# Kernel optimization log

Measured on AMD Instinct MI355X. Metric: run time of the kernel, lower is better.

The kernel has to match this reference:

```python
import jax, jax.numpy as jnp
import numpy as np

# dims: d=1024 model width, h=16 heads, d_head=64
B, S, D, H = 4, 1024, 1024, 16
RD = float(np.sqrt(D))
VAR_W_INIT = 0.001  # var_init[0]: initial weight-variance value


def setup_inputs() -> dict:
    key = jax.random.key(0)
    ks = jax.random.split(key, 5)
    x = jax.random.normal(ks[0], (B, S, D), jnp.float32)
    # input variance must be non-negative; small positive values
    var_x = jax.random.uniform(ks[1], (B, S, D), jnp.float32) * 0.01
    scale = 1.0 / np.sqrt(D)
    Wq = jax.random.normal(ks[2], (D, D), jnp.float32) * scale
    Wk = jax.random.normal(ks[3], (D, D), jnp.float32) * scale
    Wv = jax.random.normal(ks[4], (D, D), jnp.float32) * scale
    var_Wq = jnp.full((D, D), VAR_W_INIT, jnp.float32)
    var_Wk = jnp.full((D, D), VAR_W_INIT, jnp.float32)
    var_Wv = jnp.full((D, D), VAR_W_INIT, jnp.float32)
    return dict(x=x, var_x=var_x, Wq=Wq, var_Wq=var_Wq, Wk=Wk, var_Wk=var_Wk, Wv=Wv, var_Wv=var_Wv)


def _linear_vmp(x, var_x, W, var_W):
    # mean: x W^T ; variance of product of independent Gaussians:
    # var = var_x (W^2)^T + x^2 var_W^T + var_x var_W^T
    m = x @ W.T
    v = var_x @ (W * W).T + (x * x) @ var_W.T + var_x @ var_W.T
    return m, v


def _quadratic_vmp(m1, v1, m2, v2):
    # matmul of two independent Gaussian tensors (moment propagation)
    m = m1 @ m2
    v = v1 @ v2 + v1 @ (m2 * m2) + (m1 * m1) @ v2
    return m, v


def _softmax_vmp(a, var_a):
    # delta-method through softmax: J_ij = s_i(delta_ij - s_j)
    # var_i = s_i^2 [ (1-2 s_i) var_i + sum_j s_j^2 var_j ]
    s = jax.nn.softmax(a, axis=-1)
    sv = jnp.sum(s * s * var_a, axis=-1, keepdims=True)
    var_s = s * s * ((1.0 - 2.0 * s) * var_a + sv)
    return s, var_s


def _split_heads(t):
    b, s, _ = t.shape
    return t.reshape(b, s, H, D // H).transpose(0, 2, 1, 3)  # [B,H,S,dh]


def reference(x, var_x, Wq, var_Wq, Wk, var_Wk, Wv, var_Wv):
    q, vq = _linear_vmp(x, var_x, Wq, var_Wq)
    k, vk = _linear_vmp(x, var_x, Wk, var_Wk)
    v, vv = _linear_vmp(x, var_x, Wv, var_Wv)
    q, vq, k, vk, v, vv = map(_split_heads, (q, vq, k, vk, v, vv))
    kt = k.transpose(0, 1, 3, 2)
    vkt = vk.transpose(0, 1, 3, 2)
    a, va = _quadratic_vmp(q, vq, kt, vkt)          # [B,H,S,S]
    a, va = a / RD, va / (RD * RD)
    a, va = _softmax_vmp(a, va)                      # masking=False path
    o, vo = _quadratic_vmp(a, va, v, vv)             # [B,H,S,dh]
    o = o.transpose(0, 2, 1, 3).reshape(x.shape)
    vo = vo.transpose(0, 2, 1, 3).reshape(x.shape)
    # residual_vmp, mode='identity': mean add, variances add
    return x + o, var_x + vo
```

## Files before the change

kernel.cpp:

```cpp
#include <hip/hip_runtime.h>
#include <hip/hip_bf16.h>

#define BB 4
#define SS 1024
#define DD 1024
#define HH 16
#define DH 64
#define MM (BB*SS)

typedef __attribute__((ext_vector_type(8))) short bf16x8;
typedef __attribute__((ext_vector_type(8))) unsigned short u16x8;
typedef __attribute__((ext_vector_type(4))) float f32x4;

__device__ __forceinline__ float b2f(unsigned short u) {
    union { unsigned int i; float f; } c; c.i = ((unsigned int)u) << 16; return c.f;
}
__device__ __forceinline__ unsigned short f2b(float f) {
    __hip_bfloat16 h = __float2bfloat16(f);
    return *reinterpret_cast<unsigned short*>(&h);
}
__device__ __forceinline__ unsigned int pack2(float a, float b) {
    return (unsigned int)f2b(a) | ((unsigned int)f2b(b) << 16);
}
__device__ __forceinline__ void gload16(const unsigned short* g, unsigned short* l) {
    __builtin_amdgcn_global_load_lds(
        (const __attribute__((address_space(1))) void*)g,
        (__attribute__((address_space(3))) void*)l,
        16, 0, 0);
}
#define MFMA16(a, b, c) __builtin_amdgcn_mfma_f32_16x16x32_bf16(a, b, c, 0, 0, 0)

__global__ __launch_bounds__(256) void prep_x_kernel(
    const float* __restrict__ x, const float* __restrict__ vx,
    unsigned short* __restrict__ xb, unsigned short* __restrict__ vxb,
    unsigned short* __restrict__ xsb)
{
    const size_t i = ((size_t)blockIdx.x * 256 + threadIdx.x) * 4;
    float4 a = *(const float4*)(x + i);
    float4 b = *(const float4*)(vx + i);
    ushort4 oa = { f2b(a.x), f2b(a.y), f2b(a.z), f2b(a.w) };
    ushort4 ob = { f2b(b.x), f2b(b.y), f2b(b.z), f2b(b.w) };
    ushort4 os = { f2b(a.x*a.x), f2b(a.y*a.y), f2b(a.z*a.z), f2b(a.w*a.w) };
    *(ushort4*)(xb  + i) = oa;
    *(ushort4*)(vxb + i) = ob;
    *(ushort4*)(xsb + i) = os;
}

__global__ __launch_bounds__(256) void prep_w_kernel(
    const float* __restrict__ W, const float* __restrict__ vW,
    unsigned short* __restrict__ wb, unsigned short* __restrict__ wc,
    unsigned short* __restrict__ wv)
{
    const size_t i = ((size_t)blockIdx.x * 256 + threadIdx.x) * 4;
    float4 a = *(const float4*)(W + i);
    float4 b = *(const float4*)(vW + i);
    ushort4 oa = { f2b(a.x), f2b(a.y), f2b(a.z), f2b(a.w) };
    ushort4 oc = { f2b(a.x*a.x + b.x), f2b(a.y*a.y + b.y),
                   f2b(a.z*a.z + b.z), f2b(a.w*a.w + b.w) };
    ushort4 ov = { f2b(b.x), f2b(b.y), f2b(b.z), f2b(b.w) };
    *(ushort4*)(wb + i) = oa;
    *(ushort4*)(wc + i) = oc;
    *(ushort4*)(wv + i) = ov;
}

__global__ __launch_bounds__(256) void gemm_mean_kernel(
    const unsigned short* __restrict__ xb,
    const unsigned short* __restrict__ w0b, const unsigned short* __restrict__ w1b,
    const unsigned short* __restrict__ w2b,
    unsigned short* __restrict__ o0m, unsigned short* __restrict__ o1m,
    unsigned short* __restrict__ o2m)
{
    __shared__ unsigned short sA[128*32];
    __shared__ unsigned short sB[128*32];

    const int z = blockIdx.z;
    const unsigned short* Wb = (z==0)? w0b : (z==1)? w1b : w2b;
    unsigned short* Om = (z==0)? o0m : (z==1)? o1m : o2m;

    const int bn = blockIdx.x;
    const int bm = blockIdx.y;
    const int tid = threadIdx.x;
    const int w = tid >> 6;
    const int l = tid & 63;
    const int wr = w >> 1, wc = w & 1;

    const int c0 = w*64 + l;
    const int r0 = c0 >> 2, cc0 = (c0 & 3) * 8;
    const int c1 = c0 + 256;
    const int r1 = c1 >> 2, cc1 = (c1 & 3) * 8;

    const size_t aoff0 = (size_t)(bm*128 + r0) * DD + cc0;
    const size_t aoff1 = (size_t)(bm*128 + r1) * DD + cc1;
    const size_t boff0 = (size_t)(bn*128 + r0) * DD + cc0;
    const size_t boff1 = (size_t)(bn*128 + r1) * DD + cc1;

    const int lb0 = (w*64) * 8;
    const int lb1 = (256 + w*64) * 8;

    f32x4 acc[4][4];
    #pragma unroll
    for (int i = 0; i < 4; ++i)
        #pragma unroll
        for (int j = 0; j < 4; ++j)
            acc[i][j] = (f32x4){0.f,0.f,0.f,0.f};

    const int fr = l & 15;
    const int fk = (l >> 4) << 3;

    for (int kk = 0; kk < DD; kk += 32) {
        gload16(xb + aoff0 + kk, &sA[lb0]);
        gload16(xb + aoff1 + kk, &sA[lb1]);
        gload16(Wb + boff0 + kk, &sB[lb0]);
        gload16(Wb + boff1 + kk, &sB[lb1]);
        __syncthreads();

        bf16x8 bfr[4];
        #pragma unroll
        for (int j = 0; j < 4; ++j)
            bfr[j] = *(const bf16x8*)&sB[(wc*64 + j*16 + fr)*32 + fk];
        #pragma unroll
        for (int i = 0; i < 4; ++i) {
            bf16x8 a0 = *(const bf16x8*)&sA[(wr*64 + i*16 + fr)*32 + fk];
            #pragma unroll
            for (int j = 0; j < 4; ++j)
                acc[i][j] = MFMA16(a0, bfr[j], acc[i][j]);
        }
        __syncthreads();
    }

    const int orow = bm*128 + wr*64 + ((l >> 4) << 2);
    const int ocol = bn*128 + wc*64 + fr;
    #pragma unroll
    for (int i = 0; i < 4; ++i)
        #pragma unroll
        for (int j = 0; j < 4; ++j)
            #pragma unroll
            for (int r = 0; r < 4; ++r)
                Om[(size_t)(orow + i*16 + r) * DD + ocol + j*16] = f2b(acc[i][j][r]);
}

__global__ __launch_bounds__(256) void gemm_var_kernel(
    const unsigned short* __restrict__ vxb, const unsigned short* __restrict__ xsb,
    const unsigned short* __restrict__ w0c, const unsigned short* __restrict__ w0v,
    const unsigned short* __restrict__ w1c, const unsigned short* __restrict__ w1v,
    const unsigned short* __restrict__ w2c, const unsigned short* __restrict__ w2v,
    unsigned short* __restrict__ o0v, unsigned short* __restrict__ o1v,
    unsigned short* __restrict__ o2v)
{
    __shared__ unsigned short sA1[128*32];
    __shared__ unsigned short sA2[128*32];
    __shared__ unsigned short sB1[128*32];
    __shared__ unsigned short sB2[128*32];

    const int z = blockIdx.z;
    const unsigned short* Wc = (z==0)? w0c : (z==1)? w1c : w2c;
    const unsigned short* Wv = (z==0)? w0v : (z==1)? w1v : w2v;
    unsigned short* Ov = (z==0)? o0v : (z==1)? o1v : o2v;

    const int bn = blockIdx.x;
    const int bm = blockIdx.y;
    const int tid = threadIdx.x;
    const int w = tid >> 6;
    const int l = tid & 63;
    const int wr = w >> 1, wc = w & 1;

    const int c0 = w*64 + l;
    const int r0 = c0 >> 2, cc0 = (c0 & 3) * 8;
    const int c1 = c0 + 256;
    const int r1 = c1 >> 2, cc1 = (c1 & 3) * 8;

    const size_t aoff0 = (size_t)(bm*128 + r0) * DD + cc0;
    const size_t aoff1 = (size_t)(bm*128 + r1) * DD + cc1;
    const size_t boff0 = (size_t)(bn*128 + r0) * DD + cc0;
    const size_t boff1 = (size_t)(bn*128 + r1) * DD + cc1;

    const int lb0 = (w*64) * 8;
    const int lb1 = (256 + w*64) * 8;

    f32x4 acc[4][4];
    #pragma unroll
    for (int i = 0; i < 4; ++i)
        #pragma unroll
        for (int j = 0; j < 4; ++j)
            acc[i][j] = (f32x4){0.f,0.f,0.f,0.f};

    const int fr = l & 15;
    const int fk = (l >> 4) << 3;

    for (int kk = 0; kk < DD; kk += 32) {
        gload16(vxb + aoff0 + kk, &sA1[lb0]);
        gload16(vxb + aoff1 + kk, &sA1[lb1]);
        gload16(xsb + aoff0 + kk, &sA2[lb0]);
        gload16(xsb + aoff1 + kk, &sA2[lb1]);
        gload16(Wc + boff0 + kk, &sB1[lb0]);
        gload16(Wc + boff1 + kk, &sB1[lb1]);
        gload16(Wv + boff0 + kk, &sB2[lb0]);
        gload16(Wv + boff1 + kk, &sB2[lb1]);
        __syncthreads();

        bf16x8 bc[4], bv[4];
        #pragma unroll
        for (int j = 0; j < 4; ++j) {
            const int bo = (wc*64 + j*16 + fr)*32 + fk;
            bc[j] = *(const bf16x8*)&sB1[bo];
            bv[j] = *(const bf16x8*)&sB2[bo];
        }
        #pragma unroll
        for (int i = 0; i < 4; ++i) {
            const int ao = (wr*64 + i*16 + fr)*32 + fk;
            bf16x8 a1 = *(const bf16x8*)&sA1[ao];
            bf16x8 a2 = *(const bf16x8*)&sA2[ao];
            #pragma unroll
            for (int j = 0; j < 4; ++j) {
                acc[i][j] = MFMA16(a1, bc[j], acc[i][j]);
                acc[i][j] = MFMA16(a2, bv[j], acc[i][j]);
            }
        }
        __syncthreads();
    }

    const int orow = bm*128 + wr*64 + ((l >> 4) << 2);
    const int ocol = bn*128 + wc*64 + fr;
    #pragma unroll
    for (int i = 0; i < 4; ++i)
        #pragma unroll
        for (int j = 0; j < 4; ++j)
            #pragma unroll
            for (int r = 0; r < 4; ++r)
                Ov[(size_t)(orow + i*16 + r) * DD + ocol + j*16] = f2b(acc[i][j][r]);
}

__global__ __launch_bounds__(256) void prep_vt_kernel(
    const unsigned short* __restrict__ vm, const unsigned short* __restrict__ vvv,
    unsigned short* __restrict__ vt, unsigned short* __restrict__ wt,
    unsigned short* __restrict__ vvt)
{
    __shared__ unsigned short tv[64][68];
    __shared__ unsigned short tw[64][68];
    __shared__ unsigned short tvv[64][68];
    const int t = threadIdx.x;
    const int jt = blockIdx.x, h = blockIdx.y, b = blockIdx.z;
    const size_t ibase = (size_t)b*SS*DD + (size_t)h*DH;
    {
        const int j = t & 63, cg = t >> 6;
        const size_t ga = ibase + (size_t)(jt*64 + j)*DD + cg*16;
        #pragma unroll
        for (int hh = 0; hh < 2; ++hh) {
            u16x8 v8  = *(const u16x8*)(vm  + ga + hh*8);
            u16x8 vv8 = *(const u16x8*)(vvv + ga + hh*8);
            u16x8 w8;
            #pragma unroll
            for (int e = 0; e < 8; ++e) {
                float vf = b2f(v8[e]);
                w8[e] = f2b(b2f(vv8[e]) + vf*vf);
            }
            *(u16x8*)&tv[j][cg*16 + hh*8]  = v8;
            *(u16x8*)&tvv[j][cg*16 + hh*8] = vv8;
            *(u16x8*)&tw[j][cg*16 + hh*8]  = w8;
        }
    }
    __syncthreads();
    {
        const int d  = t >> 2;
        const int pc = t & 3;
        const int lc = pc ^ ((d >> 1) & 3);
        #pragma unroll
        for (int st = 0; st < 2; ++st) {
            u16x8 o0, o1, o2;
            #pragma unroll
            for (int e = 0; e < 8; ++e) {
                const int jl = st*32 + (e >> 2)*16 + lc*4 + (e & 3);
                o0[e] = tv[jl][d];
                o1[e] = tw[jl][d];
                o2[e] = tvv[jl][d];
            }
            const size_t ob = (size_t)((b*HH + h)*DH + d)*SS + jt*64 + st*32 + pc*8;
            *(u16x8*)(vt  + ob) = o0;
            *(u16x8*)(wt  + ob) = o1;
            *(u16x8*)(vvt + ob) = o2;
        }
    }
}

__global__ __launch_bounds__(256) void prep_kk_kernel(
    const unsigned short* __restrict__ kmp, const unsigned short* __restrict__ kvp,
    unsigned short* __restrict__ kkb)
{
    const size_t i = ((size_t)blockIdx.x * 256 + threadIdx.x) * 8;
    u16x8 k8 = *(const u16x8*)(kmp + i);
    u16x8 v8 = *(const u16x8*)(kvp + i);
    u16x8 o8;
    #pragma unroll
    for (int e = 0; e < 8; ++e) {
        float kf = b2f(k8[e]);
        o8[e] = f2b(b2f(v8[e]) + kf*kf);
    }
    *(u16x8*)(kkb + i) = o8;
}

union PW { unsigned int u[4]; bf16x8 v; };

__global__ __launch_bounds__(256, 3) void attn_mfma_kernel(
    const unsigned short* __restrict__ kmg, const unsigned short* __restrict__ kvg,
    const unsigned short* __restrict__ kkg,
    const unsigned short* __restrict__ vtg, const unsigned short* __restrict__ wtg,
    const unsigned short* __restrict__ vvtg,
    const unsigned short* __restrict__ qmg, const unsigned short* __restrict__ qvg,
    const float* __restrict__ x, const float* __restrict__ vx,
    float* __restrict__ om, float* __restrict__ ov)
{
    __shared__ unsigned short Ks[2][3][32*64];
    __shared__ unsigned short Vs[2][3][64*32];

    const int tid = threadIdx.x;
    const int w = tid >> 6, l = tid & 63;
    const int lo = l & 15, hi = l >> 4;

    const int fb = blockIdx.x;
    const int g  = ((fb >> 7) << 3) | (fb & 7);
    const int qt = (fb >> 3) & 15;
    const int h  = g & 15;
    const int b  = g >> 4;

    const size_t xbase = (size_t)b*SS*DD + (size_t)h*DH;
    const size_t vbase = (size_t)(b*HH + h)*DH*SS;

    bf16x8 qA[2], vqA[2], qsA[2];
    {
        const int qrow = qt*64 + w*16 + lo;
        #pragma unroll
        for (int ks = 0; ks < 2; ++ks) {
            const size_t ga = xbase + (size_t)qrow*DD + ks*32 + hi*8;
            qA[ks]  = *(const bf16x8*)(qmg + ga);
            vqA[ks] = *(const bf16x8*)(qvg + ga);
            #pragma unroll
            for (int e = 0; e < 8; ++e) {
                float f = b2f((unsigned short)qA[ks][e]);
                qsA[ks][e] = (short)f2b(f*f);
            }
        }
    }
    bf16x8 onesB;
    #pragma unroll
    for (int e = 0; e < 8; ++e) onesB[e] = (short)0x3F80;

    f32x4 T1[4], T2[4], T3[4], T4[4], T5[4];
    f32x4 zac = {0.f,0.f,0.f,0.f}, e2vac = {0.f,0.f,0.f,0.f};
    #pragma unroll
    for (int cb = 0; cb < 4; ++cb) {
        T1[cb] = (f32x4){0.f,0.f,0.f,0.f};
        T2[cb] = (f32x4){0.f,0.f,0.f,0.f};
        T3[cb] = (f32x4){0.f,0.f,0.f,0.f};
        T4[cb] = (f32x4){0.f,0.f,0.f,0.f};
        T5[cb] = (f32x4){0.f,0.f,0.f,0.f};
    }

    const size_t koff = (size_t)(l >> 3)*DD + (size_t)(((l & 7) ^ ((l >> 3) & 7)) * 8);
    const size_t voff = (size_t)(l >> 2)*SS + (size_t)((l & 3) * 8);

    const float INV_RD  = 0.03125f;
    const float INV_RD2 = 0.0009765625f;

#define IK(bu, m, p, G) gload16(G + xbase + (j0 + (size_t)(p)*8)*DD + koff, &Ks[bu][m][(p)*512])
#define IV(bu, m, p, G) gload16(G + vbase + (size_t)((p)*16)*SS + j0 + voff, &Vs[bu][m][(p)*512])
#define STAGE(tt, bu) do {                                                     \
        const size_t j0 = (size_t)(tt) * 32;                                   \
        if (w == 0)      { IK(bu,0,0,kmg); IK(bu,0,1,kmg); IK(bu,0,2,kmg);     \
                           IK(bu,0,3,kmg); IK(bu,1,0,kvg); IK(bu,1,1,kvg); }   \
        else if (w == 1) { IK(bu,1,2,kvg); IK(bu,1,3,kvg); IK(bu,2,0,kkg);     \
                           IK(bu,2,1,kkg); IK(bu,2,2,kkg); IK(bu,2,3,kkg); }   \
        else if (w == 2) { IV(bu,0,0,vtg); IV(bu,0,1,vtg); IV(bu,0,2,vtg);     \
                           IV(bu,0,3,vtg); IV(bu,1,0,wtg); IV(bu,1,1,wtg); }   \
        else             { IV(bu,1,2,wtg); IV(bu,1,3,wtg); IV(bu,2,0,vvtg);    \
                           IV(bu,2,1,vvtg); IV(bu,2,2,vvtg); IV(bu,2,3,vvtg); }\
    } while (0)

    STAGE(0, 0);
    __syncthreads();

    int cur = 0;
    for (int t = 0; t < SS/32; ++t) {
        if (t + 1 < SS/32) STAGE(t + 1, cur ^ 1);

        PW pe, pe2, pev, pe3;
        #pragma unroll
        for (int jb = 0; jb < 2; ++jb) {
            f32x4 aa = {0.f,0.f,0.f,0.f}, vva = {0.f,0.f,0.f,0.f};
            const int jrow = jb*16 + lo;
            #pragma unroll
            for (int ks = 0; ks < 2; ++ks) {
                const int co = jrow*64 + (((ks*4 + hi) ^ (lo & 7)) * 8);
                bf16x8 kB  = *(const bf16x8*)&Ks[cur][0][co];
                bf16x8 vkB = *(const bf16x8*)&Ks[cur][1][co];
                bf16x8 kkB = *(const bf16x8*)&Ks[cur][2][co];
                aa  = MFMA16(kB,  qA[ks],  aa);
                vva = MFMA16(kkB, vqA[ks], vva);
                vva = MFMA16(vkB, qsA[ks], vva);
            }
            #pragma unroll
            for (int rp = 0; rp < 2; ++rp) {
                float a0 = aa[rp*2]   * INV_RD,  va0 = vva[rp*2]   * INV_RD2;
                float a1 = aa[rp*2+1] * INV_RD,  va1 = vva[rp*2+1] * INV_RD2;
                float e0 = __expf(a0), e1 = __expf(a1);
                float s0 = e0*e0,      s1 = e1*e1;
                float v0 = s0*va0,     v1 = s1*va1;
                float t0 = v0*e0,      t1 = v1*e1;
                pe.u [jb*2+rp] = pack2(e0, e1);
                pe2.u[jb*2+rp] = pack2(s0, s1);
                pev.u[jb*2+rp] = pack2(v0, v1);
                pe3.u[jb*2+rp] = pack2(t0, t1);
            }
        }

        zac   = MFMA16(pe.v,  onesB, zac);
        e2vac = MFMA16(pev.v, onesB, e2vac);
        #pragma unroll
        for (int cb = 0; cb < 4; ++cb) {
            const int vo = (cb*16 + lo)*32 + ((hi ^ ((lo >> 1) & 3)) * 8);
            bf16x8 vB  = *(const bf16x8*)&Vs[cur][0][vo];
            bf16x8 wB  = *(const bf16x8*)&Vs[cur][1][vo];
            bf16x8 vvB = *(const bf16x8*)&Vs[cur][2][vo];
            T1[cb] = MFMA16(pe.v,  vB,  T1[cb]);
            T2[cb] = MFMA16(pev.v, wB,  T2[cb]);
            T3[cb] = MFMA16(pe3.v, wB,  T3[cb]);
            T4[cb] = MFMA16(pe2.v, wB,  T4[cb]);
            T5[cb] = MFMA16(pe2.v, vvB, T5[cb]);
        }

        __syncthreads();
        cur ^= 1;
    }

    #pragma unroll
    for (int r = 0; r < 4; ++r) {
        const float Z     = zac[r];
        const float invZ  = 1.f / Z;
        const float invZ2 = invZ * invZ;
        const float sv    = e2vac[r] * invZ2;
        const int row = qt*64 + w*16 + hi*4 + r;
        #pragma unroll
        for (int cb = 0; cb < 4; ++cb) {
            const size_t gi = xbase + (size_t)row*DD + cb*16 + lo;
            const float o  = T1[cb][r] * invZ;
            const float vo = (T2[cb][r] + sv*T4[cb][r] + T5[cb][r]) * invZ2
                           - 2.f * T3[cb][r] * invZ2 * invZ;
            om[gi] = x[gi] + o;
            ov[gi] = vx[gi] + vo;
        }
    }
#undef IK
#undef IV
#undef STAGE
}

extern "C" void kernel_launch(void* const* d_in, const int* in_sizes, int n_in,
                              void* d_out, int out_size, void* d_ws, size_t ws_size,
                              hipStream_t stream) {
    const float* x    = (const float*)d_in[0];
    const float* vx   = (const float*)d_in[1];
    const float* Wq   = (const float*)d_in[2];
    const float* vWq  = (const float*)d_in[3];
    const float* Wk   = (const float*)d_in[4];
    const float* vWk  = (const float*)d_in[5];
    const float* Wv   = (const float*)d_in[6];
    const float* vWv  = (const float*)d_in[7];

    const size_t NE = (size_t)MM * DD;
    const size_t NW = (size_t)DD * DD;

    unsigned short* u = (unsigned short*)d_ws;
    unsigned short* qm   = u + 0*NE;
    unsigned short* qv   = u + 1*NE;
    unsigned short* km   = u + 2*NE;
    unsigned short* kv   = u + 3*NE;
    unsigned short* vm   = u + 4*NE;
    unsigned short* vvv  = u + 5*NE;
    unsigned short* xbb  = u + 6*NE;
    unsigned short* vxbb = u + 7*NE;
    unsigned short* xsbb = u + 8*NE;
    unsigned short* wp   = u + 9*NE;
    unsigned short* wqb = wp + 0*NW, *wqc = wp + 1*NW, *wqv = wp + 2*NW;
    unsigned short* wkb = wp + 3*NW, *wkc = wp + 4*NW, *wkv = wp + 5*NW;
    unsigned short* wvb = wp + 6*NW, *wvc = wp + 7*NW, *wvv = wp + 8*NW;

    float* om = (float*)d_out;
    float* ov = om + NE;

    prep_x_kernel<<<4096, 256, 0, stream>>>(x, vx, xbb, vxbb, xsbb);
    prep_w_kernel<<<1024, 256, 0, stream>>>(Wq, vWq, wqb, wqc, wqv);
    prep_w_kernel<<<1024, 256, 0, stream>>>(Wk, vWk, wkb, wkc, wkv);
    prep_w_kernel<<<1024, 256, 0, stream>>>(Wv, vWv, wvb, wvc, wvv);

    dim3 gg(8, 32, 3);
    gemm_mean_kernel<<<gg, 256, 0, stream>>>(xbb, wqb, wkb, wvb, qm, km, vm);
    gemm_var_kernel<<<gg, 256, 0, stream>>>(vxbb, xsbb,
        wqc, wqv, wkc, wkv, wvc, wvv, qv, kv, vvv);

    unsigned short* vt  = xbb;
    unsigned short* wt  = vxbb;
    unsigned short* vvt = xsbb;
    unsigned short* kkb = wp;
    dim3 gt(SS/64, HH, BB);
    prep_vt_kernel<<<gt, 256, 0, stream>>>(vm, vvv, vt, wt, vvt);
    prep_kk_kernel<<<2048, 256, 0, stream>>>(km, kv, kkb);

    attn_mfma_kernel<<<1024, 256, 0, stream>>>(km, kv, kkb, vt, wt, vvt,
                                               qm, qv, x, vx, om, ov);
}
```

Before: 245.4 us.

## Merge mean/variance projection GEMMs into one double-buffered swizzled kernel

Replaces the separate mean and variance projection GEMM kernels with a single kernel launched over six z-slices. The variance slices run as one GEMM with a doubled K loop that walks both operand pairs in sequence. The K loop now uses double-buffered LDS so the next tile's global loads overlap the current tile's MFMAs, and an XOR swizzle on LDS columns is meant to reduce bank conflicts. The three weight-prep launches are also merged into one grid, which cuts launch count and lets mean and variance blocks share the GPU, at the cost of uneven block lengths within the grid.

```diff
diff --git a/kernel.cpp b/kernel.cpp
--- a/kernel.cpp
+++ b/kernel.cpp
@@ -47,10 +47,19 @@
 }
 
 __global__ __launch_bounds__(256) void prep_w_kernel(
-    const float* __restrict__ W, const float* __restrict__ vW,
-    unsigned short* __restrict__ wb, unsigned short* __restrict__ wc,
-    unsigned short* __restrict__ wv)
-{
+    const float* __restrict__ W0, const float* __restrict__ vW0,
+    const float* __restrict__ W1, const float* __restrict__ vW1,
+    const float* __restrict__ W2, const float* __restrict__ vW2,
+    unsigned short* __restrict__ wp)
+{
+    const int z = blockIdx.y;
+    const float* W  = (z==0)? W0 : (z==1)? W1 : W2;
+    const float* vW = (z==0)? vW0: (z==1)? vW1: vW2;
+    const size_t NW = (size_t)DD*DD;
+    unsigned short* wb = wp + (size_t)(3*z+0)*NW;
+    unsigned short* wc = wp + (size_t)(3*z+1)*NW;
+    unsigned short* wv = wp + (size_t)(3*z+2)*NW;
+
     const size_t i = ((size_t)blockIdx.x * 256 + threadIdx.x) * 4;
     float4 a = *(const float4*)(W + i);
     float4 b = *(const float4*)(vW + i);
@@ -63,19 +72,29 @@
     *(ushort4*)(wv + i) = ov;
 }
 
-__global__ __launch_bounds__(256) void gemm_mean_kernel(
-    const unsigned short* __restrict__ xb,
-    const unsigned short* __restrict__ w0b, const unsigned short* __restrict__ w1b,
-    const unsigned short* __restrict__ w2b,
-    unsigned short* __restrict__ o0m, unsigned short* __restrict__ o1m,
-    unsigned short* __restrict__ o2m)
-{
-    __shared__ unsigned short sA[128*32];
-    __shared__ unsigned short sB[128*32];
+__global__ __launch_bounds__(256) void gemm_proj_kernel(
+    const unsigned short* __restrict__ xb, const unsigned short* __restrict__ vxb,
+    const unsigned short* __restrict__ xsb,
+    const unsigned short* __restrict__ wp,
+    unsigned short* __restrict__ qm, unsigned short* __restrict__ km,
+    unsigned short* __restrict__ vm,
+    unsigned short* __restrict__ qv, unsigned short* __restrict__ kv,
+    unsigned short* __restrict__ vvv)
+{
+    __shared__ unsigned short sA[2][128*32];
+    __shared__ unsigned short sB[2][128*32];
 
     const int z = blockIdx.z;
-    const unsigned short* Wb = (z==0)? w0b : (z==1)? w1b : w2b;
-    unsigned short* Om = (z==0)? o0m : (z==1)? o1m : o2m;
+    const size_t NW = (size_t)DD*DD;
+    const bool isVar = (z >= 3);
+    const int p = isVar ? (z - 3) : z;
+    const unsigned short* A0 = isVar ? vxb : xb;
+    const unsigned short* A1 = isVar ? xsb : xb;
+    const unsigned short* B0 = wp + (size_t)(3*p + (isVar ? 1 : 0)) * NW;
+    const unsigned short* B1 = isVar ? (wp + (size_t)(3*p + 2) * NW) : B0;
+    unsigned short* Out = (z==0)? qm : (z==1)? km : (z==2)? vm
+                        : (z==3)? qv : (z==4)? kv : vvv;
+    const int NT = isVar ? 64 : 32;
 
     const int bn = blockIdx.x;
     const int bm = blockIdx.y;
@@ -84,18 +103,22 @@
     const int l = tid & 63;
     const int wr = w >> 1, wc = w & 1;
 
-    const int c0 = w*64 + l;
-    const int r0 = c0 >> 2, cc0 = (c0 & 3) * 8;
-    const int c1 = c0 + 256;
-    const int r1 = c1 >> 2, cc1 = (c1 & 3) * 8;
-
-    const size_t aoff0 = (size_t)(bm*128 + r0) * DD + cc0;
-    const size_t aoff1 = (size_t)(bm*128 + r1) * DD + cc1;
-    const size_t boff0 = (size_t)(bn*128 + r0) * DD + cc0;
-    const size_t boff1 = (size_t)(bn*128 + r1) * DD + cc1;
-
-    const int lb0 = (w*64) * 8;
-    const int lb1 = (256 + w*64) * 8;
+    const int r0 = tid >> 2;
+    const int s0 = (((tid & 3) ^ ((r0 >> 1) & 3)) * 8);
+    const size_t aoff0 = (size_t)(bm*128 + r0) * DD + s0;
+    const size_t boff0 = (size_t)(bn*128 + r0) * DD + s0;
+    const int ldsd0 = (w*64) * 8;
+    const int ldsd1 = (256 + w*64) * 8;
+
+#define STG(buf, t) do {                                                   \
+        const unsigned short* As_ = ((t) < 32) ? A0 : A1;                  \
+        const unsigned short* Bs_ = ((t) < 32) ? B0 : B1;                  \
+        const int kc_ = ((t) & 31) * 32;                                   \
+        gload16(As_ + aoff0 + kc_,                   &sA[buf][ldsd0]);     \
+        gload16(As_ + aoff0 + (size_t)64*DD + kc_,   &sA[buf][ldsd1]);     \
+        gload16(Bs_ + boff0 + kc_,                   &sB[buf][ldsd0]);     \
+        gload16(Bs_ + boff0 + (size_t)64*DD + kc_,   &sB[buf][ldsd1]);     \
+    } while (0)
 
     f32x4 acc[4][4];
     #pragma unroll
@@ -105,30 +128,34 @@
             acc[i][j] = (f32x4){0.f,0.f,0.f,0.f};
 
     const int fr = l & 15;
-    const int fk = (l >> 4) << 3;
-
-    for (int kk = 0; kk < DD; kk += 32) {
-        gload16(xb + aoff0 + kk, &sA[lb0]);
-        gload16(xb + aoff1 + kk, &sA[lb1]);
-        gload16(Wb + boff0 + kk, &sB[lb0]);
-        gload16(Wb + boff1 + kk, &sB[lb1]);
-        __syncthreads();
+    const int hi = l >> 4;
+
+    STG(0, 0);
+    __syncthreads();
+
+    for (int t = 0; t < NT; ++t) {
+        const int cb = t & 1;
+        if (t + 1 < NT) STG(cb ^ 1, t + 1);
 
         bf16x8 bfr[4];
         #pragma unroll
-        for (int j = 0; j < 4; ++j)
-            bfr[j] = *(const bf16x8*)&sB[(wc*64 + j*16 + fr)*32 + fk];
+        for (int j = 0; j < 4; ++j) {
+            const int row = wc*64 + j*16 + fr;
+            bfr[j] = *(const bf16x8*)&sB[cb][row*32 + ((hi ^ ((row >> 1) & 3)) * 8)];
+        }
         #pragma unroll
         for (int i = 0; i < 4; ++i) {
-            bf16x8 a0 = *(const bf16x8*)&sA[(wr*64 + i*16 + fr)*32 + fk];
+            const int row = wr*64 + i*16 + fr;
+            bf16x8 a0 = *(const bf16x8*)&sA[cb][row*32 + ((hi ^ ((row >> 1) & 3)) * 8)];
             #pragma unroll
             for (int j = 0; j < 4; ++j)
                 acc[i][j] = MFMA16(a0, bfr[j], acc[i][j]);
         }
         __syncthreads();
     }
-
-    const int orow = bm*128 + wr*64 + ((l >> 4) << 2);
+#undef STG
+
+    const int orow = bm*128 + wr*64 + (hi << 2);
     const int ocol = bn*128 + wc*64 + fr;
     #pragma unroll
     for (int i = 0; i < 4; ++i)
@@ -136,98 +163,7 @@
         for (int j = 0; j < 4; ++j)
             #pragma unroll
             for (int r = 0; r < 4; ++r)
-                Om[(size_t)(orow + i*16 + r) * DD + ocol + j*16] = f2b(acc[i][j][r]);
-}
-
-__global__ __launch_bounds__(256) void gemm_var_kernel(
-    const unsigned short* __restrict__ vxb, const unsigned short* __restrict__ xsb,
-    const unsigned short* __restrict__ w0c, const unsigned short* __restrict__ w0v,
-    const unsigned short* __restrict__ w1c, const unsigned short* __restrict__ w1v,
-    const unsigned short* __restrict__ w2c, const unsigned short* __restrict__ w2v,
-    unsigned short* __restrict__ o0v, unsigned short* __restrict__ o1v,
-    unsigned short* __restrict__ o2v)
-{
-    __shared__ unsigned short sA1[128*32];
-    __shared__ unsigned short sA2[128*32];
-    __shared__ unsigned short sB1[128*32];
-    __shared__ unsigned short sB2[128*32];
-
-    const int z = blockIdx.z;
-    const unsigned short* Wc = (z==0)? w0c : (z==1)? w1c : w2c;
-    const unsigned short* Wv = (z==0)? w0v : (z==1)? w1v : w2v;
-    unsigned short* Ov = (z==0)? o0v : (z==1)? o1v : o2v;
-
-    const int bn = blockIdx.x;
-    const int bm = blockIdx.y;
-    const int tid = threadIdx.x;
-    const int w = tid >> 6;
-    const int l = tid & 63;
-    const int wr = w >> 1, wc = w & 1;
-
-    const int c0 = w*64 + l;
-    const int r0 = c0 >> 2, cc0 = (c0 & 3) * 8;
-    const int c1 = c0 + 256;
-    const int r1 = c1 >> 2, cc1 = (c1 & 3) * 8;
-
-    const size_t aoff0 = (size_t)(bm*128 + r0) * DD + cc0;
-    const size_t aoff1 = (size_t)(bm*128 + r1) * DD + cc1;
-    const size_t boff0 = (size_t)(bn*128 + r0) * DD + cc0;
-    const size_t boff1 = (size_t)(bn*128 + r1) * DD + cc1;
-
-    const int lb0 = (w*64) * 8;
-    const int lb1 = (256 + w*64) * 8;
-
-    f32x4 acc[4][4];
-    #pragma unroll
-    for (int i = 0; i < 4; ++i)
-        #pragma unroll
-        for (int j = 0; j < 4; ++j)
-            acc[i][j] = (f32x4){0.f,0.f,0.f,0.f};
-
-    const int fr = l & 15;
-    const int fk = (l >> 4) << 3;
-
-    for (int kk = 0; kk < DD; kk += 32) {
-        gload16(vxb + aoff0 + kk, &sA1[lb0]);
-        gload16(vxb + aoff1 + kk, &sA1[lb1]);
-        gload16(xsb + aoff0 + kk, &sA2[lb0]);
-        gload16(xsb + aoff1 + kk, &sA2[lb1]);
-        gload16(Wc + boff0 + kk, &sB1[lb0]);
-        gload16(Wc + boff1 + kk, &sB1[lb1]);
-        gload16(Wv + boff0 + kk, &sB2[lb0]);
-        gload16(Wv + boff1 + kk, &sB2[lb1]);
-        __syncthreads();
-
-        bf16x8 bc[4], bv[4];
-        #pragma unroll
-        for (int j = 0; j < 4; ++j) {
-            const int bo = (wc*64 + j*16 + fr)*32 + fk;
-            bc[j] = *(const bf16x8*)&sB1[bo];
-            bv[j] = *(const bf16x8*)&sB2[bo];
-        }
-        #pragma unroll
-        for (int i = 0; i < 4; ++i) {
-            const int ao = (wr*64 + i*16 + fr)*32 + fk;
-            bf16x8 a1 = *(const bf16x8*)&sA1[ao];
-            bf16x8 a2 = *(const bf16x8*)&sA2[ao];
-            #pragma unroll
-            for (int j = 0; j < 4; ++j) {
-                acc[i][j] = MFMA16(a1, bc[j], acc[i][j]);
-                acc[i][j] = MFMA16(a2, bv[j], acc[i][j]);
-            }
-        }
-        __syncthreads();
-    }
-
-    const int orow = bm*128 + wr*64 + ((l >> 4) << 2);
-    const int ocol = bn*128 + wc*64 + fr;
-    #pragma unroll
-    for (int i = 0; i < 4; ++i)
-        #pragma unroll
-        for (int j = 0; j < 4; ++j)
-            #pragma unroll
-            for (int r = 0; r < 4; ++r)
-                Ov[(size_t)(orow + i*16 + r) * DD + ocol + j*16] = f2b(acc[i][j][r]);
+                Out[(size_t)(orow + i*16 + r) * DD + ocol + j*16] = f2b(acc[i][j][r]);
 }
 
 __global__ __launch_bounds__(256) void prep_vt_kernel(
@@ -479,22 +415,16 @@
     unsigned short* vxbb = u + 7*NE;
     unsigned short* xsbb = u + 8*NE;
     unsigned short* wp   = u + 9*NE;
-    unsigned short* wqb = wp + 0*NW, *wqc = wp + 1*NW, *wqv = wp + 2*NW;
-    unsigned short* wkb = wp + 3*NW, *wkc = wp + 4*NW, *wkv = wp + 5*NW;
-    unsigned short* wvb = wp + 6*NW, *wvc = wp + 7*NW, *wvv = wp + 8*NW;
 
     float* om = (float*)d_out;
     float* ov = om + NE;
 
     prep_x_kernel<<<4096, 256, 0, stream>>>(x, vx, xbb, vxbb, xsbb);
-    prep_w_kernel<<<1024, 256, 0, stream>>>(Wq, vWq, wqb, wqc, wqv);
-    prep_w_kernel<<<1024, 256, 0, stream>>>(Wk, vWk, wkb, wkc, wkv);
-    prep_w_kernel<<<1024, 256, 0, stream>>>(Wv, vWv, wvb, wvc, wvv);
-
-    dim3 gg(8, 32, 3);
-    gemm_mean_kernel<<<gg, 256, 0, stream>>>(xbb, wqb, wkb, wvb, qm, km, vm);
-    gemm_var_kernel<<<gg, 256, 0, stream>>>(vxbb, xsbb,
-        wqc, wqv, wkc, wkv, wvc, wvv, qv, kv, vvv);
+    prep_w_kernel<<<dim3(1024, 3), 256, 0, stream>>>(Wq, vWq, Wk, vWk, Wv, vWv, wp);
+
+    dim3 gg(8, 32, 6);
+    gemm_proj_kernel<<<gg, 256, 0, stream>>>(xbb, vxbb, xsbb, wp,
+                                             qm, km, vm, qv, kv, vvv);
 
     unsigned short* vt  = xbb;
     unsigned short* wt  = vxbb;
```

Result: faster. 204.6 us (-16.6%).
